# Kernel tuning notes

Hardware: AMD Instinct MI355X
Metric: run time of the kernel (lower is better)

Reference implementation:

```python
import jax, jax.numpy as jnp
import numpy as np

DIM = 2048
N_HEADS = 32
N_KV_HEADS = 8
HEAD_DIM = 64
REPEATS = N_HEADS // N_KV_HEADS
SCALE = HEAD_DIM ** -0.5
L = 2048
B = 1


def rotary_matrix(context_len, d):
    # Dense (L, d, d) RoPE rotation matrix, exactly as get_rotary_matrix1.
    pos = jnp.arange(1, context_len + 1, dtype=jnp.float32)[:, None]
    i = jnp.arange(d // 2)
    theta = 10000.0 ** (-2.0 * i.astype(jnp.float32) / d)
    m_theta = pos * theta  # (L, d/2)
    cos_v, sin_v = jnp.cos(m_theta), jnp.sin(m_theta)
    R = jnp.zeros((context_len, d, d), dtype=jnp.float32)
    R = R.at[:, 2 * i, 2 * i].set(cos_v)
    R = R.at[:, 2 * i, 2 * i + 1].set(-sin_v)
    R = R.at[:, 2 * i + 1, 2 * i].set(sin_v)
    R = R.at[:, 2 * i + 1, 2 * i + 1].set(cos_v)
    return R


def causal_mask(context_len):
    idx = jnp.arange(context_len)
    return (idx[:, None] < idx[None, :]).astype(jnp.float32) * -1e9


def setup_inputs() -> dict:
    key = jax.random.key(0)
    ks = jax.random.split(key, 5)
    x = jax.random.normal(ks[0], (B, L, DIM), dtype=jnp.float32)
    mask = causal_mask(L)
    wq_w = jax.random.normal(ks[1], (N_HEADS * HEAD_DIM, DIM), dtype=jnp.float32) * 0.02
    wk_w = jax.random.normal(ks[2], (N_KV_HEADS * HEAD_DIM, DIM), dtype=jnp.float32) * 0.02
    wv_w = jax.random.normal(ks[3], (N_KV_HEADS * HEAD_DIM, DIM), dtype=jnp.float32) * 0.02
    wo_w = jax.random.normal(ks[4], (DIM, N_HEADS * HEAD_DIM), dtype=jnp.float32) * 0.02
    return {"x": x, "mask": mask, "wq_w": wq_w, "wk_w": wk_w, "wv_w": wv_w, "wo_w": wo_w}


def reference(x, mask, wq_w, wk_w, wv_w, wo_w):
    Bx, Lx, D = x.shape
    # projections (torch Linear: y = x @ W.T)
    q = jnp.einsum('bld,od->blo', x, wq_w).reshape(Bx, Lx, N_HEADS, HEAD_DIM).transpose(0, 2, 1, 3)
    k = jnp.einsum('bld,od->blo', x, wk_w).reshape(Bx, Lx, N_KV_HEADS, HEAD_DIM).transpose(0, 2, 1, 3)
    v = jnp.einsum('bld,od->blo', x, wv_w).reshape(Bx, Lx, N_KV_HEADS, HEAD_DIM).transpose(0, 2, 1, 3)
    # GQA repeat of kv heads (interleaved, matching concat-unsqueeze-reshape)
    k = jnp.repeat(k, REPEATS, axis=1)
    v = jnp.repeat(v, REPEATS, axis=1)
    # dense-matrix RoPE on q and (repeated) k
    R = rotary_matrix(Lx, HEAD_DIM)
    q = jnp.einsum('bhlj,lij->bhli', q, R)
    k = jnp.einsum('bhlj,lij->bhli', k, R)
    scores = jnp.einsum('bhld,bhmd->bhlm', q, k) * SCALE + mask
    attn = jax.nn.softmax(scores.astype(jnp.float32), axis=-1)
    out = jnp.einsum('bhlm,bhmd->bhld', attn, v)
    out = out.transpose(0, 2, 1, 3).reshape(Bx, Lx, N_HEADS * HEAD_DIM)
    out = jnp.einsum('blo,do->bld', out, wo_w)
    return out, k, v
```

## Files before the change

### kernel.cpp

```cpp
#include <hip/hip_runtime.h>

typedef __bf16 bf16;
typedef __bf16 bf16x8 __attribute__((ext_vector_type(8)));
typedef float floatx4 __attribute__((ext_vector_type(4)));
typedef float floatx16 __attribute__((ext_vector_type(16)));
typedef unsigned int uint;

#define MFMA16(a, b, c) __builtin_amdgcn_mfma_f32_16x16x32_bf16((a), (b), (c), 0, 0, 0)
#define MFMA32(a, b, c) __builtin_amdgcn_mfma_f32_32x32x16_bf16((a), (b), (c), 0, 0, 0)

__device__ __forceinline__ void gl2lds16(const bf16* g, bf16* l) {
  __builtin_amdgcn_global_load_lds(
      (const __attribute__((address_space(1))) void*)g,
      (__attribute__((address_space(3))) void*)l, 16, 0, 0);
}
__device__ __forceinline__ void wait_vm0() { __builtin_amdgcn_s_waitcnt(0x0f70); }

__device__ __forceinline__ void cvt8(const float* __restrict__ s,
                                     bf16* __restrict__ d, int i8) {
  const float4 a = ((const float4*)s)[i8 * 2];
  const float4 b = ((const float4*)s)[i8 * 2 + 1];
  bf16x8 o;
  o[0] = (bf16)a.x; o[1] = (bf16)a.y; o[2] = (bf16)a.z; o[3] = (bf16)a.w;
  o[4] = (bf16)b.x; o[5] = (bf16)b.y; o[6] = (bf16)b.z; o[7] = (bf16)b.w;
  *(bf16x8*)(d + i8 * 8) = o;
}

__global__ __launch_bounds__(256) void convert_kernel(
    const float* __restrict__ x, const float* __restrict__ wq,
    const float* __restrict__ wk, const float* __restrict__ wv,
    const float* __restrict__ wo, bf16* __restrict__ xb,
    bf16* __restrict__ wqb, bf16* __restrict__ wkb, bf16* __restrict__ wvb,
    bf16* __restrict__ wob) {
  const int g = blockIdx.x * 256 + threadIdx.x;
  if (g < 524288) cvt8(x, xb, g);
  else if (g < 1048576) cvt8(wq, wqb, g - 524288);
  else if (g < 1179648) cvt8(wk, wkb, g - 1048576);
  else if (g < 1310720) cvt8(wv, wvb, g - 1179648);
  else cvt8(wo, wob, g - 1310720);
}

template <typename OutT>
__device__ __forceinline__ void gemm_tile_body64(
    const bf16* __restrict__ A, int lda,
    const bf16* __restrict__ B, int ldb,
    OutT* __restrict__ C, int ldc, int K,
    bf16* S) {
  const int t = threadIdx.x;
  const int w = t >> 6, lane = t & 63;
  const int l15 = lane & 15, qd = lane >> 4;
  const int wr = w >> 1, wc = w & 1;

  floatx4 acc[2][4];
#pragma unroll
  for (int i = 0; i < 2; ++i)
#pragma unroll
    for (int j = 0; j < 4; ++j) acc[i][j] = (floatx4){0.f, 0.f, 0.f, 0.f};

  const bf16* gb[6];
  int lo[6];
#pragma unroll
  for (int i = 0; i < 6; ++i) {
    const int u = w + 4 * i;
    lo[i] = u * 512 + lane * 8;
    if (u < 8) {
      gb[i] = A + ((u >> 1) * 16 + l15) * lda + (u & 1) * 32 + qd * 8;
    } else {
      const int v = u - 8;
      gb[i] = B + ((v >> 1) * 16 + l15) * ldb + (v & 1) * 32 + qd * 8;
    }
  }

#define STG64(kt_, buf_)                                            \
  {                                                                 \
    bf16* d_ = S + (buf_) * 12288;                                  \
    _Pragma("unroll")                                               \
    for (int i_ = 0; i_ < 6; ++i_)                                  \
      gl2lds16(gb[i_] + (kt_) * 64, d_ + lo[i_]);                   \
  }

  const int NT = K >> 6;
  STG64(0, 0);
  wait_vm0();
  __syncthreads();
  int cur = 0;
  for (int kt = 0; kt < NT; ++kt) {
    if (kt + 1 < NT) STG64(kt + 1, cur ^ 1);
    const bf16* Ab = S + cur * 12288;
    const bf16* Bb = Ab + 4096;
    bf16x8 a[2][2], b[4][2];
#pragma unroll
    for (int i = 0; i < 2; ++i)
#pragma unroll
      for (int kk = 0; kk < 2; ++kk)
        a[i][kk] =
            *(const bf16x8*)(Ab + ((wr * 2 + i) * 2 + kk) * 512 + lane * 8);
#pragma unroll
    for (int j = 0; j < 4; ++j)
#pragma unroll
      for (int kk = 0; kk < 2; ++kk)
        b[j][kk] =
            *(const bf16x8*)(Bb + ((wc * 4 + j) * 2 + kk) * 512 + lane * 8);
#pragma unroll
    for (int kk = 0; kk < 2; ++kk)
#pragma unroll
      for (int i = 0; i < 2; ++i)
#pragma unroll
        for (int j = 0; j < 4; ++j)
          acc[i][j] = MFMA16(a[i][kk], b[j][kk], acc[i][j]);
    wait_vm0();
    __builtin_amdgcn_sched_barrier(0);
    __builtin_amdgcn_s_barrier();
    __builtin_amdgcn_sched_barrier(0);
    cur ^= 1;
  }
#undef STG64

#pragma unroll
  for (int i = 0; i < 2; ++i)
#pragma unroll
    for (int j = 0; j < 4; ++j) {
      const int row = wr * 32 + i * 16 + qd * 4;
      const int col = wc * 64 + j * 16 + l15;
#pragma unroll
      for (int r = 0; r < 4; ++r)
        C[(row + r) * ldc + col] = (OutT)acc[i][j][r];
    }
}

__global__ __launch_bounds__(256) void gemm_qkv(
    const bf16* __restrict__ x, const bf16* __restrict__ wq,
    const bf16* __restrict__ wk, const bf16* __restrict__ wv,
    bf16* __restrict__ Qws, bf16* __restrict__ Kws, bf16* __restrict__ Vws) {
  __shared__ bf16 S[24576];
  const int m0 = blockIdx.y * 64;
  const int nb = blockIdx.x;
  const bf16* B;
  bf16* C;
  int ldc;
  if (nb < 16) {
    B = wq + nb * 128 * 2048;
    C = Qws + m0 * 2048 + nb * 128;
    ldc = 2048;
  } else if (nb < 20) {
    B = wk + (nb - 16) * 128 * 2048;
    C = Kws + m0 * 512 + (nb - 16) * 128;
    ldc = 512;
  } else {
    B = wv + (nb - 20) * 128 * 2048;
    C = Vws + m0 * 512 + (nb - 20) * 128;
    ldc = 512;
  }
  gemm_tile_body64<bf16>(x + m0 * 2048, 2048, B, 2048, C, ldc, 2048, S);
}

__global__ __launch_bounds__(256) void gemm_o(
    const bf16* __restrict__ Ows, const bf16* __restrict__ wo,
    float* __restrict__ out) {
  __shared__ bf16 S[24576];
  const int m0 = blockIdx.y * 64, n0 = blockIdx.x * 128;
  gemm_tile_body64<float>(Ows + m0 * 2048, 2048, wo + n0 * 2048, 2048,
                          out + m0 * 2048 + n0, 2048, 2048, S);
}

__global__ __launch_bounds__(256) void rope_repeat_kernel(
    bf16* __restrict__ Qws, bf16* __restrict__ Kws, bf16* __restrict__ Kh,
    const bf16* __restrict__ Vws, bf16* __restrict__ Vt,
    float* __restrict__ kout, float* __restrict__ vout) {
  const int gid = blockIdx.x * 256 + threadIdx.x;
  const float NEG_LOG2_10000_D32 = -0.4152410118609203f;
  if (gid < 2097152) {
    const int l = gid >> 10, pr = gid & 1023, a = pr & 31;
    bf16* p = Qws + l * 2048 + pr * 2;
    const float x0 = (float)p[0], x1 = (float)p[1];
    const float ang = (float)(l + 1) * exp2f(NEG_LOG2_10000_D32 * (float)a);
    float s, c;
    __sincosf(ang, &s, &c);
    p[0] = (bf16)(c * x0 - s * x1);
    p[1] = (bf16)(s * x0 + c * x1);
  } else if (gid < 2097152 + 524288) {
    const int g = gid - 2097152;
    const int l = g >> 8, pr = g & 255, a = pr & 31, kvh = pr >> 5;
    bf16* p = Kws + l * 512 + pr * 2;
    const float x0 = (float)p[0], x1 = (float)p[1];
    const float ang = (float)(l + 1) * exp2f(NEG_LOG2_10000_D32 * (float)a);
    float s, c;
    __sincosf(ang, &s, &c);
    const float y0 = c * x0 - s * x1;
    const float y1 = s * x0 + c * x1;
    p[0] = (bf16)y0;
    p[1] = (bf16)y1;
    bf16* kp = Kh + (kvh * 2048 + l) * 64 + a * 2;
    kp[0] = (bf16)y0;
    kp[1] = (bf16)y1;
#pragma unroll
    for (int rep = 0; rep < 4; ++rep) {
      float* o = kout + (((kvh * 4 + rep) * 2048 + l) * 64 + a * 2);
      o[0] = y0;
      o[1] = y1;
    }
  } else if (gid < 2097152 + 524288 + 131072) {
    const int c = gid - (2097152 + 524288);
    const int l = c >> 6, seg = c & 63, kvh = seg >> 3;
    const bf16x8 v = *(const bf16x8*)(Vws + l * 512 + seg * 8);
    float4 f0, f1;
    f0.x = (float)v[0]; f0.y = (float)v[1]; f0.z = (float)v[2]; f0.w = (float)v[3];
    f1.x = (float)v[4]; f1.y = (float)v[5]; f1.z = (float)v[6]; f1.w = (float)v[7];
#pragma unroll
    for (int rep = 0; rep < 4; ++rep) {
      float* o = vout + (((kvh * 4 + rep) * 2048 + l) * 64 + (seg & 7) * 8);
      *(float4*)o = f0;
      *(float4*)(o + 4) = f1;
    }
  } else {
    const int c = gid - (2097152 + 524288 + 131072);
    const int kvh = c >> 14, r2 = c & 16383, dseg = r2 >> 11, l = r2 & 2047;
    const int d0 = dseg * 8;
    const bf16x8 v = *(const bf16x8*)(Vws + l * 512 + kvh * 64 + d0);
#pragma unroll
    for (int jj = 0; jj < 8; ++jj)
      Vt[kvh * 131072 + (d0 + jj) * 2048 + l] = v[jj];
  }
}

__global__ __launch_bounds__(256) void flash_kernel(
    const bf16* __restrict__ Qws, const bf16* __restrict__ Kh,
    const bf16* __restrict__ Vt, bf16* __restrict__ Ows,
    float* __restrict__ Opart, float* __restrict__ ML) {
  __shared__ bf16 KVs[2][2][4096];
  __shared__ bf16 Osh[128 * 66];

  const int h = blockIdx.y;
  const int bx = blockIdx.x;
  int qt, seg, kts, kte;
  if (bx < 8) {
    qt = bx; seg = -1; kts = 0; kte = 2 * qt + 2;
  } else {
    const int i = bx - 8;
    qt = 8 + (i >> 1);
    seg = i & 1;
    const int half = qt + 1;
    kts = seg * half;
    kte = kts + half;
  }
  const int kh = h >> 2;
  const int q0 = qt * 128;
  const int t = threadIdx.x, w = t >> 6, lane = t & 63;
  const int l31 = lane & 31, hf = lane >> 5;
  const int qw = q0 + w * 32;

  bf16x8 qf[4];
  {
    const bf16* qrow = Qws + (qw + l31) * 2048 + h * 64 + hf * 8;
#pragma unroll
    for (int c = 0; c < 4; ++c) qf[c] = *(const bf16x8*)(qrow + c * 16);
  }

  floatx16 o[2] = {};
  float mrun = -3e38f, lrun = 0.f;

  const int s0 = w, s1 = w + 4;
  const bf16* gK0 = Kh + kh * 131072 + ((s0 >> 2) * 32 + l31) * 64 + (s0 & 3) * 16 + hf * 8;
  const bf16* gK1 = Kh + kh * 131072 + ((s1 >> 2) * 32 + l31) * 64 + (s1 & 3) * 16 + hf * 8;
  const bf16* gV0 = Vt + kh * 131072 + ((s0 >> 2) * 32 + l31) * 2048 + (s0 & 3) * 16 + hf * 8;
  const bf16* gV1 = Vt + kh * 131072 + ((s1 >> 2) * 32 + l31) * 2048 + (s1 & 3) * 16 + hf * 8;

  {
    const int nb = kts & 1;
    gl2lds16(gK0 + kts * 4096, &KVs[nb][0][s0 * 512 + lane * 8]);
    gl2lds16(gK1 + kts * 4096, &KVs[nb][0][s1 * 512 + lane * 8]);
    gl2lds16(gV0 + kts * 64, &KVs[nb][1][s0 * 512 + lane * 8]);
    gl2lds16(gV1 + kts * 64, &KVs[nb][1][s1 * 512 + lane * 8]);
  }

  const float C = 0.1803368801f;
  for (int kt = kts; kt < kte; ++kt) {
    wait_vm0();
    __syncthreads();
    if (kt + 1 < kte) {
      const int nb = (kt + 1) & 1;
      const int koff = (kt + 1) * 4096, voff = (kt + 1) * 64;
      gl2lds16(gK0 + koff, &KVs[nb][0][s0 * 512 + lane * 8]);
      gl2lds16(gK1 + koff, &KVs[nb][0][s1 * 512 + lane * 8]);
      gl2lds16(gV0 + voff, &KVs[nb][1][s0 * 512 + lane * 8]);
      gl2lds16(gV1 + voff, &KVs[nb][1][s1 * 512 + lane * 8]);
    }
    const int kt64 = kt * 64;
    if (kt64 > qw + 31) continue;
    const bf16* Kb = &KVs[kt & 1][0][0];
    const bf16* Vb = &KVs[kt & 1][1][0];

    floatx16 st[2];
    __builtin_amdgcn_s_setprio(1);
#pragma unroll
    for (int tt = 0; tt < 2; ++tt) {
      floatx16 z = {};
#pragma unroll
      for (int c = 0; c < 4; ++c) {
        const bf16x8 kf = *(const bf16x8*)(Kb + (tt * 4 + c) * 512 + lane * 8);
        z = MFMA32(kf, qf[c], z);
      }
      st[tt] = z;
    }
    __builtin_amdgcn_s_setprio(0);
    if (kt64 + 64 > qw) {
      const int myq = qw + l31;
#pragma unroll
      for (int tt = 0; tt < 2; ++tt)
#pragma unroll
        for (int r = 0; r < 16; ++r) {
          const int key = kt64 + tt * 32 + (r & 3) + 8 * (r >> 2) + 4 * hf;
          if (key > myq) st[tt][r] = -1e30f;
        }
    }
    float ma = -3e38f, mb = -3e38f, mc = -3e38f, md = -3e38f;
#pragma unroll
    for (int tt = 0; tt < 2; ++tt)
#pragma unroll
      for (int r = 0; r < 16; r += 4) {
        ma = fmaxf(ma, st[tt][r + 0]);
        mb = fmaxf(mb, st[tt][r + 1]);
        mc = fmaxf(mc, st[tt][r + 2]);
        md = fmaxf(md, st[tt][r + 3]);
      }
    float mx = fmaxf(fmaxf(ma, mb), fmaxf(mc, md));
    mx = fmaxf(mx, __shfl_xor(mx, 32));
    const bool defer = __all((mx - mrun) * C <= 8.f);
    if (!defer) {
      const float mn = fmaxf(mrun, mx);
      const float al = __builtin_amdgcn_exp2f((mrun - mn) * C);
      lrun *= al;
#pragma unroll
      for (int n = 0; n < 2; ++n)
#pragma unroll
        for (int r = 0; r < 16; ++r) o[n][r] *= al;
      mrun = mn;
    }
    float ra = 0.f, rb = 0.f, rc = 0.f, rd = 0.f;
#pragma unroll
    for (int tt = 0; tt < 2; ++tt)
#pragma unroll
      for (int r = 0; r < 16; r += 4) {
        const float p0 = __builtin_amdgcn_exp2f((st[tt][r + 0] - mrun) * C);
        const float p1 = __builtin_amdgcn_exp2f((st[tt][r + 1] - mrun) * C);
        const float p2 = __builtin_amdgcn_exp2f((st[tt][r + 2] - mrun) * C);
        const float p3 = __builtin_amdgcn_exp2f((st[tt][r + 3] - mrun) * C);
        st[tt][r + 0] = p0; ra += p0;
        st[tt][r + 1] = p1; rb += p1;
        st[tt][r + 2] = p2; rc += p2;
        st[tt][r + 3] = p3; rd += p3;
      }
    float rs = (ra + rb) + (rc + rd);
    rs += __shfl_xor(rs, 32);
    lrun += rs;

    uint pk[2][4][2];
#pragma unroll
    for (int tt = 0; tt < 2; ++tt)
#pragma unroll
      for (int g = 0; g < 4; ++g)
#pragma unroll
        for (int p = 0; p < 2; ++p) {
          union { bf16 h2[2]; uint u; } cv;
          cv.h2[0] = (bf16)st[tt][4 * g + 2 * p];
          cv.h2[1] = (bf16)st[tt][4 * g + 2 * p + 1];
          pk[tt][g][p] = cv.u;
        }
    uint own_[2][2][2], rv[2][2][2];
#pragma unroll
    for (int tt = 0; tt < 2; ++tt)
#pragma unroll
      for (int gam = 0; gam < 2; ++gam)
#pragma unroll
        for (int p = 0; p < 2; ++p) {
          own_[tt][gam][p] = hf ? pk[tt][2 * gam + 1][p] : pk[tt][2 * gam][p];
          const uint snd = hf ? pk[tt][2 * gam][p] : pk[tt][2 * gam + 1][p];
          rv[tt][gam][p] = (uint)__shfl_xor((int)snd, 32);
        }
    __builtin_amdgcn_s_setprio(1);
#pragma unroll
    for (int c = 0; c < 4; ++c) {
      const int tt = c >> 1, gam = c & 1;
      union { uint u[4]; bf16x8 v; } pf;
      pf.u[0] = hf ? rv[tt][gam][0] : own_[tt][gam][0];
      pf.u[1] = hf ? rv[tt][gam][1] : own_[tt][gam][1];
      pf.u[2] = hf ? own_[tt][gam][0] : rv[tt][gam][0];
      pf.u[3] = hf ? own_[tt][gam][1] : rv[tt][gam][1];
#pragma unroll
      for (int n = 0; n < 2; ++n)
        o[n] = MFMA32(*(const bf16x8*)(Vb + (n * 4 + c) * 512 + lane * 8),
                      pf.v, o[n]);
    }
    __builtin_amdgcn_s_setprio(0);
  }

  if (seg < 0) {
    const float inv = 1.f / lrun;
#pragma unroll
    for (int n = 0; n < 2; ++n)
#pragma unroll
      for (int r = 0; r < 16; ++r) {
        const int dl = n * 32 + (r & 3) + 8 * (r >> 2) + 4 * hf;
        Osh[(w * 32 + l31) * 66 + dl] = (bf16)(o[n][r] * inv);
      }
    __syncthreads();
#pragma unroll
    for (int i = 0; i < 4; ++i) {
      const int row = (t >> 3) + i * 32;
      const int col = (t & 7) * 8;
      const bf16x8 vv = *(const bf16x8*)&Osh[row * 66 + col];
      *(bf16x8*)&Ows[(q0 + row) * 2048 + h * 64 + col] = vv;
    }
  } else {
    const int idx = (h * 8 + (qt - 8)) * 2 + seg;
    float* Op = Opart + idx * 8192;
#pragma unroll
    for (int n = 0; n < 2; ++n)
#pragma unroll
      for (int r = 0; r < 16; ++r) {
        const int dl = n * 32 + (r & 3) + 8 * (r >> 2) + 4 * hf;
        Op[dl * 128 + w * 32 + l31] = o[n][r];
      }
    if (hf == 0) {
      ML[idx * 256 + w * 32 + l31] = mrun;
      ML[idx * 256 + 128 + w * 32 + l31] = lrun;
    }
  }
}

__global__ __launch_bounds__(256) void combine_kernel(
    const float* __restrict__ Opart, const float* __restrict__ ML,
    bf16* __restrict__ Ows) {
  __shared__ bf16 Osh[128 * 66];
  const int b = blockIdx.x;
  const int h = b >> 3, qt = (b & 7) + 8;
  const int q0 = qt * 128;
  const int t = threadIdx.x;
  const int row = t & 127, dh = t >> 7;
  const int i0 = (h * 8 + (qt - 8)) * 2;
  const float C = 0.1803368801f;
  const float m0 = ML[i0 * 256 + row], l0 = ML[i0 * 256 + 128 + row];
  const float m1 = ML[(i0 + 1) * 256 + row], l1 = ML[(i0 + 1) * 256 + 128 + row];
  const float m = fmaxf(m0, m1);
  const float w0 = __builtin_amdgcn_exp2f((m0 - m) * C);
  const float w1 = __builtin_amdgcn_exp2f((m1 - m) * C);
  const float inv = 1.f / (l0 * w0 + l1 * w1);
  const float* P0 = Opart + i0 * 8192;
  const float* P1 = Opart + (i0 + 1) * 8192;
#pragma unroll
  for (int j = 0; j < 32; ++j) {
    const int d = dh * 32 + j;
    const float v = (P0[d * 128 + row] * w0 + P1[d * 128 + row] * w1) * inv;
    Osh[row * 66 + d] = (bf16)v;
  }
  __syncthreads();
#pragma unroll
  for (int i = 0; i < 4; ++i) {
    const int r2 = (t >> 3) + i * 32;
    const int col = (t & 7) * 8;
    const bf16x8 vv = *(const bf16x8*)&Osh[r2 * 66 + col];
    *(bf16x8*)&Ows[(q0 + r2) * 2048 + h * 64 + col] = vv;
  }
}

extern "C" void kernel_launch(void* const* d_in, const int* in_sizes, int n_in,
                              void* d_out, int out_size, void* d_ws,
                              size_t ws_size, hipStream_t stream) {
  const float* x = (const float*)d_in[0];
  const float* wq = (const float*)d_in[2];
  const float* wk = (const float*)d_in[3];
  const float* wv = (const float*)d_in[4];
  const float* wo = (const float*)d_in[5];

  float* out = (float*)d_out;
  float* kout = out + 4194304;
  float* vout = out + 8388608;

  bf16* ws = (bf16*)d_ws;
  bf16* xb = ws;
  bf16* wqb = xb + 4194304;
  bf16* wkb = wqb + 4194304;
  bf16* wvb = wkb + 1048576;
  bf16* wob = wvb + 1048576;
  bf16* Qws = wob + 4194304;
  bf16* Kws = Qws + 4194304;
  bf16* Vws = Kws + 1048576;
  bf16* Vt = Vws + 1048576;
  bf16* Ows = Vt + 1048576;
  bf16* Kh = Ows + 4194304;
  float* Opart = out;
  float* MLf = (float*)Kws;

  convert_kernel<<<dim3(7168), dim3(256), 0, stream>>>(x, wq, wk, wv, wo, xb,
                                                       wqb, wkb, wvb, wob);
  gemm_qkv<<<dim3(24, 32), dim3(256), 0, stream>>>(xb, wqb, wkb, wvb, Qws, Kws,
                                                   Vws);
  rope_repeat_kernel<<<dim3(11264), dim3(256), 0, stream>>>(Qws, Kws, Kh, Vws,
                                                            Vt, kout, vout);
  flash_kernel<<<dim3(24, 32), dim3(256), 0, stream>>>(Qws, Kh, Vt, Ows, Opart,
                                                       MLf);
  combine_kernel<<<dim3(256), dim3(256), 0, stream>>>(Opart, MLf, Ows);
  gemm_o<<<dim3(16, 32), dim3(256), 0, stream>>>(Ows, wob, out);
}
```

Before: 297.7 us.

## Split-K QKV projection with 128x128 tiles and separate fp32 combine pass

```diff
diff --git a/kernel.cpp b/kernel.cpp
--- a/kernel.cpp
+++ b/kernel.cpp
@@ -41,6 +41,68 @@
 }
 
 template <typename OutT>
+__device__ __forceinline__ void gemm_tile_body32(
+    const bf16* __restrict__ A, int lda,
+    const bf16* __restrict__ B, int ldb,
+    OutT* __restrict__ C, int ldc, int K,
+    bf16* As, bf16* Bs) {
+  const int t = threadIdx.x;
+  const int w = t >> 6, lane = t & 63;
+  const int l15 = lane & 15, qd = lane >> 4;
+  const int wr = w >> 1, wc = w & 1;
+
+  floatx4 acc[4][4];
+#pragma unroll
+  for (int i = 0; i < 4; ++i)
+#pragma unroll
+    for (int j = 0; j < 4; ++j) acc[i][j] = (floatx4){0.f, 0.f, 0.f, 0.f};
+
+  const int mt0 = w, mt1 = w + 4;
+  const int kseg = qd * 8;
+  const bf16* ga0 = A + (mt0 * 16 + l15) * lda + kseg;
+  const bf16* ga1 = A + (mt1 * 16 + l15) * lda + kseg;
+  const bf16* gb0 = B + (mt0 * 16 + l15) * ldb + kseg;
+  const bf16* gb1 = B + (mt1 * 16 + l15) * ldb + kseg;
+  bf16* lA0 = As + mt0 * 512 + lane * 8;
+  bf16* lA1 = As + mt1 * 512 + lane * 8;
+  bf16* lB0 = Bs + mt0 * 512 + lane * 8;
+  bf16* lB1 = Bs + mt1 * 512 + lane * 8;
+
+  for (int k0 = 0; k0 < K; k0 += 32) {
+    gl2lds16(ga0 + k0, lA0);
+    gl2lds16(ga1 + k0, lA1);
+    gl2lds16(gb0 + k0, lB0);
+    gl2lds16(gb1 + k0, lB1);
+    wait_vm0();
+    __syncthreads();
+
+    bf16x8 a[4], b[4];
+#pragma unroll
+    for (int i = 0; i < 4; ++i)
+      a[i] = *(const bf16x8*)(As + (wr * 4 + i) * 512 + lane * 8);
+#pragma unroll
+    for (int j = 0; j < 4; ++j)
+      b[j] = *(const bf16x8*)(Bs + (wc * 4 + j) * 512 + lane * 8);
+#pragma unroll
+    for (int i = 0; i < 4; ++i)
+#pragma unroll
+      for (int j = 0; j < 4; ++j) acc[i][j] = MFMA16(a[i], b[j], acc[i][j]);
+    __syncthreads();
+  }
+
+#pragma unroll
+  for (int i = 0; i < 4; ++i)
+#pragma unroll
+    for (int j = 0; j < 4; ++j) {
+      const int row = wr * 64 + i * 16 + qd * 4;
+      const int col = wc * 64 + j * 16 + l15;
+#pragma unroll
+      for (int r = 0; r < 4; ++r)
+        C[(row + r) * ldc + col] = (OutT)acc[i][j][r];
+    }
+}
+
+template <typename OutT>
 __device__ __forceinline__ void gemm_tile_body64(
     const bf16* __restrict__ A, int lda,
     const bf16* __restrict__ B, int ldb,
@@ -131,27 +193,41 @@
 __global__ __launch_bounds__(256) void gemm_qkv(
     const bf16* __restrict__ x, const bf16* __restrict__ wq,
     const bf16* __restrict__ wk, const bf16* __restrict__ wv,
-    bf16* __restrict__ Qws, bf16* __restrict__ Kws, bf16* __restrict__ Vws) {
-  __shared__ bf16 S[24576];
-  const int m0 = blockIdx.y * 64;
+    float* __restrict__ P) {
+  __shared__ bf16 As[4096], Bs[4096];
+  const int m0 = blockIdx.y * 128;
   const int nb = blockIdx.x;
+  const int s = blockIdx.z;
   const bf16* B;
-  bf16* C;
-  int ldc;
-  if (nb < 16) {
-    B = wq + nb * 128 * 2048;
-    C = Qws + m0 * 2048 + nb * 128;
-    ldc = 2048;
-  } else if (nb < 20) {
-    B = wk + (nb - 16) * 128 * 2048;
-    C = Kws + m0 * 512 + (nb - 16) * 128;
-    ldc = 512;
-  } else {
-    B = wv + (nb - 20) * 128 * 2048;
-    C = Vws + m0 * 512 + (nb - 20) * 128;
-    ldc = 512;
-  }
-  gemm_tile_body64<bf16>(x + m0 * 2048, 2048, B, 2048, C, ldc, 2048, S);
+  if (nb < 16) B = wq + nb * 128 * 2048;
+  else if (nb < 20) B = wk + (nb - 16) * 128 * 2048;
+  else B = wv + (nb - 20) * 128 * 2048;
+  float* C = P + s * 6291456 + m0 * 3072 + nb * 128;
+  gemm_tile_body32<float>(x + m0 * 2048 + s * 1024, 2048, B + s * 1024, 2048,
+                          C, 3072, 1024, As, Bs);
+}
+
+__global__ __launch_bounds__(256) void combine_qkv(
+    const float* __restrict__ P, bf16* __restrict__ Qws,
+    bf16* __restrict__ Kws, bf16* __restrict__ Vws) {
+  const int g = blockIdx.x * 256 + threadIdx.x;
+  const int base = g * 8;
+  const int row = base / 3072;
+  const int col = base - row * 3072;
+  const float4 a0 = *(const float4*)(P + base);
+  const float4 a1 = *(const float4*)(P + base + 4);
+  const float4 b0 = *(const float4*)(P + 6291456 + base);
+  const float4 b1 = *(const float4*)(P + 6291456 + base + 4);
+  bf16x8 o;
+  o[0] = (bf16)(a0.x + b0.x); o[1] = (bf16)(a0.y + b0.y);
+  o[2] = (bf16)(a0.z + b0.z); o[3] = (bf16)(a0.w + b0.w);
+  o[4] = (bf16)(a1.x + b1.x); o[5] = (bf16)(a1.y + b1.y);
+  o[6] = (bf16)(a1.z + b1.z); o[7] = (bf16)(a1.w + b1.w);
+  bf16* dst;
+  if (col < 2048) dst = Qws + row * 2048 + col;
+  else if (col < 2560) dst = Kws + row * 512 + (col - 2048);
+  else dst = Vws + row * 512 + (col - 2560);
+  *(bf16x8*)dst = o;
 }
 
 __global__ __launch_bounds__(256) void gemm_o(
@@ -488,13 +564,14 @@
   bf16* Vt = Vws + 1048576;
   bf16* Ows = Vt + 1048576;
   bf16* Kh = Ows + 4194304;
+  float* Pqkv = out;
   float* Opart = out;
   float* MLf = (float*)Kws;
 
   convert_kernel<<<dim3(7168), dim3(256), 0, stream>>>(x, wq, wk, wv, wo, xb,
                                                        wqb, wkb, wvb, wob);
-  gemm_qkv<<<dim3(24, 32), dim3(256), 0, stream>>>(xb, wqb, wkb, wvb, Qws, Kws,
-                                                   Vws);
+  gemm_qkv<<<dim3(24, 16, 2), dim3(256), 0, stream>>>(xb, wqb, wkb, wvb, Pqkv);
+  combine_qkv<<<dim3(3072), dim3(256), 0, stream>>>(Pqkv, Qws, Kws, Vws);
   rope_repeat_kernel<<<dim3(11264), dim3(256), 0, stream>>>(Qws, Kws, Kh, Vws,
                                                             Vt, kout, vout);
   flash_kernel<<<dim3(24, 32), dim3(256), 0, stream>>>(Qws, Kh, Vt, Ows, Opart,
```

Measured after the change: 307.5 us. +3.3%, slower.
